# Kernel tuning notes

Hardware: AMD Instinct MI355X
Metric: run time of the kernel (lower is better)

## Reference

```python
import jax, jax.numpy as jnp
import numpy as np

H, W = 8, 64
HK, WK = 7, 11
N = H * W            # 512 tokens
C = 512              # embed_dim
HEADS = 8
HD = C // HEADS      # 64
SCALE = HD ** -0.5
B = 32


def build_local_mask():
    # Faithful port of the build() mask construction.
    m = np.ones([N, H + HK - 1, W + WK - 1], dtype=np.int32)
    for h in range(H):
        for w in range(W):
            m[h * W + w, h:h + HK, w:w + WK] = 0
    m = m[:, HK // 2:H + HK // 2, WK // 2:W + WK // 2].reshape(-1, N).astype(bool)
    mask = np.where(m, -1e30, 0.0).astype(np.float32)
    return jnp.asarray(mask.reshape(1, 1, N, N))


def setup_inputs() -> dict:
    key = jax.random.key(0)
    k1, k2, k3, k4 = jax.random.split(key, 4)
    return {
        "x": jax.random.normal(k1, (B, N, C), dtype=jnp.float32),
        "w_qkv": jax.random.normal(k2, (C, 3 * C), dtype=jnp.float32) * (C ** -0.5),
        "w_proj": jax.random.normal(k3, (C, C), dtype=jnp.float32) * (C ** -0.5),
        "b_proj": jax.random.normal(k4, (C,), dtype=jnp.float32) * 0.01,
        "mask": build_local_mask(),
    }


def reference(x, w_qkv, w_proj, b_proj, mask):
    b = x.shape[0]
    qkv = x @ w_qkv                                   # [B, N, 3C]
    qkv = qkv.reshape(b, N, 3, HEADS, HD)
    qkv = jnp.transpose(qkv, (2, 0, 3, 1, 4))          # [3, B, heads, N, hd]
    q, k, v = qkv[0], qkv[1], qkv[2]
    attn = jnp.einsum("bhnd,bhmd->bhnm", q * SCALE, k) + mask  # [B, heads, N, N]
    attn = jax.nn.softmax(attn, axis=-1)
    out = jnp.einsum("bhnm,bhmd->bhnd", attn, v)       # [B, heads, N, hd]
    out = jnp.transpose(out, (0, 2, 1, 3)).reshape(b, N, C)
    return out @ w_proj + b_proj
```

## Files before the change

### kernel.cpp

```cpp
#include <hip/hip_runtime.h>
#include <hip/hip_bf16.h>

typedef __attribute__((ext_vector_type(8))) __bf16 bf16x8;
typedef __attribute__((ext_vector_type(4))) float f32x4;

__device__ __forceinline__ unsigned short f2bf(float f) {
    unsigned int u = __float_as_uint(f);
    unsigned int r = u + 0x7FFFu + ((u >> 16) & 1u);
    return (unsigned short)(r >> 16);
}

__device__ __forceinline__ void async_copy16(const unsigned short* g, unsigned short* l) {
    __builtin_amdgcn_global_load_lds(
        (__attribute__((address_space(1))) void*)(g),
        (__attribute__((address_space(3))) void*)(l), 16, 0, 0);
}

__global__ __launch_bounds__(256) void cvt_f32_bf16(const float4* __restrict__ in,
                                                    uint4* __restrict__ out, int n8) {
    int i = blockIdx.x * blockDim.x + threadIdx.x;
    if (i >= n8) return;
    float4 a = in[2 * i], b = in[2 * i + 1];
    union { unsigned short s[8]; uint4 v; } r;
    r.s[0] = f2bf(a.x); r.s[1] = f2bf(a.y); r.s[2] = f2bf(a.z); r.s[3] = f2bf(a.w);
    r.s[4] = f2bf(b.x); r.s[5] = f2bf(b.y); r.s[6] = f2bf(b.z); r.s[7] = f2bf(b.w);
    out[i] = r.v;
}

__global__ __launch_bounds__(256) void transpose_cvt(const float* __restrict__ in,
                                                     unsigned short* __restrict__ out,
                                                     int R, int C) {
    __shared__ float tile[32][33];
    int c0 = blockIdx.x * 32, r0 = blockIdx.y * 32;
    int tx = threadIdx.x, ty = threadIdx.y;
    #pragma unroll
    for (int i = 0; i < 32; i += 8)
        tile[ty + i][tx] = in[(size_t)(r0 + ty + i) * C + c0 + tx];
    __syncthreads();
    #pragma unroll
    for (int i = 0; i < 32; i += 8)
        out[(size_t)(c0 + ty + i) * R + r0 + tx] = f2bf(tile[tx][ty + i]);
}

template <int K>
__device__ __forceinline__ void gemm_core_128_db(const unsigned short* __restrict__ A,
                                                 const unsigned short* __restrict__ Bt,
                                                 int m0, int n0, f32x4 acc[4][4]) {
    __shared__ unsigned short As[2][128 * 64];
    __shared__ unsigned short Bs[2][128 * 64];
    const int tid = threadIdx.x;
    const int lane = tid & 63;
    const int wv   = tid >> 6;
    const int wm = (wv >> 1) * 64, wn = (wv & 1) * 64;
    const int l15 = lane & 15, l16 = lane >> 4;

    f32x4 zz = {0.f, 0.f, 0.f, 0.f};
    #pragma unroll
    for (int i = 0; i < 4; ++i)
        #pragma unroll
        for (int j = 0; j < 4; ++j) acc[i][j] = zz;

    const int r_st  = tid >> 3;
    const int kk_st = (tid & 7) * 8;
    const unsigned short* Arow = A  + (size_t)(m0 + r_st) * K + kk_st;
    const unsigned short* Brow = Bt + (size_t)(n0 + r_st) * K + kk_st;

    #pragma unroll
    for (int c = 0; c < 4; ++c) {
        int flat16 = c * 256 + tid;
        async_copy16(Arow + (size_t)c * 32 * K, As[0] + flat16 * 8);
        async_copy16(Brow + (size_t)c * 32 * K, Bs[0] + flat16 * 8);
    }
    __syncthreads();

    constexpr int NT = K >> 6;
    #pragma unroll
    for (int t = 0; t < NT; ++t) {
        const int cur = t & 1;
        if (t + 1 < NT) {
            const int k0 = (t + 1) << 6;
            #pragma unroll
            for (int c = 0; c < 4; ++c) {
                int flat16 = c * 256 + tid;
                async_copy16(Arow + (size_t)c * 32 * K + k0, As[cur ^ 1] + flat16 * 8);
                async_copy16(Brow + (size_t)c * 32 * K + k0, Bs[cur ^ 1] + flat16 * 8);
            }
        }
        #pragma unroll
        for (int kk = 0; kk < 64; kk += 32) {
            bf16x8 a[4], b[4];
            #pragma unroll
            for (int i = 0; i < 4; ++i)
                a[i] = *(const bf16x8*)(const void*)(As[cur] + (wm + i * 16 + l15) * 64 + kk + l16 * 8);
            #pragma unroll
            for (int i = 0; i < 4; ++i)
                b[i] = *(const bf16x8*)(const void*)(Bs[cur] + (wn + i * 16 + l15) * 64 + kk + l16 * 8);
            #pragma unroll
            for (int i = 0; i < 4; ++i)
                #pragma unroll
                for (int j = 0; j < 4; ++j)
                    acc[i][j] = __builtin_amdgcn_mfma_f32_16x16x32_bf16(a[i], b[j], acc[i][j], 0, 0, 0);
        }
        __syncthreads();
    }
}

__global__ __launch_bounds__(256) void gemm_qkv(const unsigned short* __restrict__ xb,
                                                const unsigned short* __restrict__ wT,
                                                unsigned short* __restrict__ Qb,
                                                unsigned short* __restrict__ Kb,
                                                unsigned short* __restrict__ Vb) {
    f32x4 acc[4][4];
    int m0 = blockIdx.y * 128, n0 = blockIdx.x * 128;
    gemm_core_128_db<512>(xb, wT, m0, n0, acc);
    const int lane = threadIdx.x & 63, wv = threadIdx.x >> 6;
    const int wm = (wv >> 1) * 64, wn = (wv & 1) * 64;
    const int l15 = lane & 15, l16 = lane >> 4;
    #pragma unroll
    for (int j = 0; j < 4; ++j) {
        int col = n0 + wn + j * 16 + l15;
        int t = col >> 9;
        int within = col & 511;
        int h = within >> 6, d = within & 63;
        unsigned short* dst = (t == 0) ? Qb : (t == 1) ? Kb : Vb;
        float scl = (t == 0) ? 0.125f : 1.0f;
        #pragma unroll
        for (int i = 0; i < 4; ++i)
            #pragma unroll
            for (int e = 0; e < 4; ++e) {
                int row = m0 + wm + i * 16 + (l16 << 2) + e;
                int b = row >> 9, n = row & 511;
                dst[(((size_t)b * 8 + h) * 512 + n) * 64 + d] = f2bf(acc[i][j][e] * scl);
            }
    }
}

__global__ __launch_bounds__(256, 4) void attn_kernel(const unsigned short* __restrict__ Qb,
                                                      const unsigned short* __restrict__ Kb,
                                                      const unsigned short* __restrict__ Vb,
                                                      unsigned short* __restrict__ Ob) {
    __shared__ unsigned short Ks[64 * 72];
    __shared__ unsigned short Vt[64 * 72];
    __shared__ unsigned short Ps[4 * 32 * 72];

    const int bh = blockIdx.x >> 2;
    const int qt = blockIdx.x & 3;
    const int tid = threadIdx.x;
    const int lane = tid & 63;
    const int wv = tid >> 6;
    const int l15 = lane & 15, l16 = lane >> 4;
    const int b = bh >> 3, h = bh & 7;

    const unsigned short* Qp = Qb + (size_t)bh * 512 * 64;
    const unsigned short* Kp = Kb + (size_t)bh * 512 * 64;
    const unsigned short* Vp = Vb + (size_t)bh * 512 * 64;
    unsigned short* Pw = Ps + wv * 32 * 72;

    const int qrow0 = qt * 128 + wv * 32;
    const int qh = qrow0 >> 6;
    const int wq0 = qrow0 & 63;
    const int dead_g = wq0 ? 0 : 3;

    unsigned int wbits = 0;
    {
        int qw[2] = { wq0 + l15, wq0 + 16 + l15 };
        #pragma unroll
        for (int qf = 0; qf < 2; ++qf)
            #pragma unroll
            for (int g = 0; g < 4; ++g)
                #pragma unroll
                for (int j = 0; j < 4; ++j) {
                    int kw = g * 16 + (l16 << 2) + j;
                    int dw = qw[qf] - kw; dw = dw < 0 ? -dw : dw;
                    wbits |= (dw <= 5 ? 1u : 0u) << (qf * 16 + g * 4 + j);
                }
    }

    bf16x8 bQ[2][2];
    #pragma unroll
    for (int qf = 0; qf < 2; ++qf)
        #pragma unroll
        for (int kf = 0; kf < 2; ++kf)
            bQ[qf][kf] = *(const bf16x8*)(const void*)(Qp + (size_t)(qrow0 + qf * 16 + l15) * 64 + kf * 32 + l16 * 8);

    f32x4 o[2][4];
    f32x4 zz = {0.f, 0.f, 0.f, 0.f};
    float mrow[2] = {-INFINITY, -INFINITY}, lrow[2] = {0.f, 0.f};
    #pragma unroll
    for (int qf = 0; qf < 2; ++qf)
        #pragma unroll
        for (int df = 0; df < 4; ++df) o[qf][df] = zz;

    for (int kh = 0; kh < 8; ++kh) {
        int dlo = kh - 2 * qt;
        if (dlo < -3 || dlo > 4) continue;
        __syncthreads();
        #pragma unroll
        for (int c = 0; c < 2; ++c) {
            int flat16 = c * 256 + tid;
            int key = flat16 >> 3, dk = (flat16 & 7) * 8;
            *(uint4*)(void*)(Ks + key * 72 + dk) = *(const uint4*)(const void*)(Kp + ((size_t)(kh * 64 + key) * 64 + dk));
        }
        #pragma unroll
        for (int c = 0; c < 2; ++c) {
            int flat16 = c * 256 + tid;
            int key = flat16 & 63, d8 = flat16 >> 6;
            union { uint4 v; unsigned short s[8]; } t;
            t.v = *(const uint4*)(const void*)(Vp + ((size_t)(kh * 64 + key) * 64 + d8 * 8));
            #pragma unroll
            for (int e = 0; e < 8; ++e) Vt[(d8 * 8 + e) * 72 + key] = t.s[e];
        }
        __syncthreads();

        int adq = qh - kh; adq = adq < 0 ? -adq : adq;
        if (adq > 3) continue;

        f32x4 s[2][4];
        #pragma unroll
        for (int qf = 0; qf < 2; ++qf)
            #pragma unroll
            for (int g = 0; g < 4; ++g) s[qf][g] = zz;
        #pragma unroll
        for (int g = 0; g < 4; ++g) {
            if (g == dead_g) continue;
            bf16x8 aK0 = *(const bf16x8*)(const void*)(Ks + (g * 16 + l15) * 72 + 0  + l16 * 8);
            bf16x8 aK1 = *(const bf16x8*)(const void*)(Ks + (g * 16 + l15) * 72 + 32 + l16 * 8);
            #pragma unroll
            for (int qf = 0; qf < 2; ++qf) {
                s[qf][g] = __builtin_amdgcn_mfma_f32_16x16x32_bf16(aK0, bQ[qf][0], s[qf][g], 0, 0, 0);
                s[qf][g] = __builtin_amdgcn_mfma_f32_16x16x32_bf16(aK1, bQ[qf][1], s[qf][g], 0, 0, 0);
            }
        }

        float tmax[2] = {-1e30f, -1e30f};
        #pragma unroll
        for (int qf = 0; qf < 2; ++qf) {
            #pragma unroll
            for (int g = 0; g < 4; ++g) {
                if (g == dead_g) continue;
                #pragma unroll
                for (int j = 0; j < 4; ++j) {
                    float v = ((wbits >> (qf * 16 + g * 4 + j)) & 1u) ? s[qf][g][j] : -1e30f;
                    s[qf][g][j] = v;
                    tmax[qf] = fmaxf(tmax[qf], v);
                }
            }
            float t = tmax[qf];
            t = fmaxf(t, __shfl_xor(t, 16));
            t = fmaxf(t, __shfl_xor(t, 32));
            tmax[qf] = t;
        }

        #pragma unroll
        for (int qf = 0; qf < 2; ++qf) {
            float mnew = fmaxf(mrow[qf], tmax[qf]);
            float fs = __expf(mrow[qf] - mnew);
            mrow[qf] = mnew;
            lrow[qf] *= fs;
            #pragma unroll
            for (int j = 0; j < 4; ++j) {
                float fso = __shfl(fs, (l16 << 2) + j);
                #pragma unroll
                for (int df = 0; df < 4; ++df) o[qf][df][j] *= fso;
            }
        }

        #pragma unroll
        for (int qf = 0; qf < 2; ++qf) {
            float lsum = 0.f;
            #pragma unroll
            for (int g = 0; g < 4; ++g) {
                unsigned int lo, hi;
                if (g == dead_g) {
                    lo = 0u; hi = 0u;
                } else {
                    float e0 = __expf(s[qf][g][0] - mrow[qf]);
                    float e1 = __expf(s[qf][g][1] - mrow[qf]);
                    float e2 = __expf(s[qf][g][2] - mrow[qf]);
                    float e3 = __expf(s[qf][g][3] - mrow[qf]);
                    lsum += (e0 + e1) + (e2 + e3);
                    asm("v_cvt_pk_bf16_f32 %0, %1, %2" : "=v"(lo) : "v"(e0), "v"(e1));
                    asm("v_cvt_pk_bf16_f32 %0, %1, %2" : "=v"(hi) : "v"(e2), "v"(e3));
                }
                uint2 w; w.x = lo; w.y = hi;
                *(uint2*)(void*)(Pw + (qf * 16 + l15) * 72 + g * 16 + (l16 << 2)) = w;
            }
            float t = lsum;
            t += __shfl_xor(t, 16);
            t += __shfl_xor(t, 32);
            lrow[qf] += t;
        }
        asm volatile("" ::: "memory");

        #pragma unroll
        for (int kf = 0; kf < 2; ++kf) {
            bf16x8 aP0 = *(const bf16x8*)(const void*)(Pw + (0 * 16 + l15) * 72 + kf * 32 + l16 * 8);
            bf16x8 aP1 = *(const bf16x8*)(const void*)(Pw + (1 * 16 + l15) * 72 + kf * 32 + l16 * 8);
            #pragma unroll
            for (int df = 0; df < 4; ++df) {
                bf16x8 bV = *(const bf16x8*)(const void*)(Vt + (df * 16 + l15) * 72 + kf * 32 + l16 * 8);
                o[0][df] = __builtin_amdgcn_mfma_f32_16x16x32_bf16(aP0, bV, o[0][df], 0, 0, 0);
                o[1][df] = __builtin_amdgcn_mfma_f32_16x16x32_bf16(aP1, bV, o[1][df], 0, 0, 0);
            }
        }
    }

    #pragma unroll
    for (int qf = 0; qf < 2; ++qf) {
        float linv = 1.0f / lrow[qf];
        #pragma unroll
        for (int j = 0; j < 4; ++j) {
            float lj = __shfl(linv, (l16 << 2) + j);
            int q = qrow0 + qf * 16 + (l16 << 2) + j;
            size_t base = ((size_t)b * 512 + q) * 512 + h * 64;
            #pragma unroll
            for (int df = 0; df < 4; ++df)
                Ob[base + df * 16 + l15] = f2bf(o[qf][df][j] * lj);
        }
    }
}

__global__ __launch_bounds__(256) void gemm_proj(const unsigned short* __restrict__ Ab,
                                                 const unsigned short* __restrict__ wT,
                                                 const float* __restrict__ bias,
                                                 float* __restrict__ out) {
    f32x4 acc[4][4];
    int m0 = blockIdx.y * 128, n0 = blockIdx.x * 128;
    gemm_core_128_db<512>(Ab, wT, m0, n0, acc);
    const int lane = threadIdx.x & 63, wv = threadIdx.x >> 6;
    const int wm = (wv >> 1) * 64, wn = (wv & 1) * 64;
    const int l15 = lane & 15, l16 = lane >> 4;
    #pragma unroll
    for (int j = 0; j < 4; ++j) {
        int col = n0 + wn + j * 16 + l15;
        float bb = bias[col];
        #pragma unroll
        for (int i = 0; i < 4; ++i)
            #pragma unroll
            for (int e = 0; e < 4; ++e) {
                int row = m0 + wm + i * 16 + (l16 << 2) + e;
                out[(size_t)row * 512 + col] = acc[i][j][e] + bb;
            }
    }
}

extern "C" void kernel_launch(void* const* d_in, const int* in_sizes, int n_in,
                              void* d_out, int out_size, void* d_ws, size_t ws_size,
                              hipStream_t stream) {
    const float* x      = (const float*)d_in[0];
    const float* w_qkv  = (const float*)d_in[1];
    const float* w_proj = (const float*)d_in[2];
    const float* b_proj = (const float*)d_in[3];
    float* out = (float*)d_out;

    char* ws = (char*)d_ws;
    unsigned short* xb     = (unsigned short*)(ws);
    unsigned short* wqkvT  = (unsigned short*)(ws + 16777216);
    unsigned short* wprojT = (unsigned short*)(ws + 18350080);
    unsigned short* Qb     = (unsigned short*)(ws + 18874368);
    unsigned short* Kb     = (unsigned short*)(ws + 35651584);
    unsigned short* Vb     = (unsigned short*)(ws + 52428800);
    unsigned short* Ob     = xb;

    cvt_f32_bf16<<<4096, 256, 0, stream>>>((const float4*)x, (uint4*)xb, 1048576);
    transpose_cvt<<<dim3(48, 16), dim3(32, 8), 0, stream>>>(w_qkv, wqkvT, 512, 1536);
    transpose_cvt<<<dim3(16, 16), dim3(32, 8), 0, stream>>>(w_proj, wprojT, 512, 512);
    gemm_qkv<<<dim3(12, 128), 256, 0, stream>>>(xb, wqkvT, Qb, Kb, Vb);
    attn_kernel<<<1024, 256, 0, stream>>>(Qb, Kb, Vb, Ob);
    gemm_proj<<<dim3(4, 128), 256, 0, stream>>>(Ob, wprojT, b_proj, out);
}
```

Baseline: 114.6 us.

## Use 256x128 GEMM tiles with 8 waves, XCD-aware block mapping, interleaved prefetch

Both projection GEMMs now use one shared core with 256x128 tiles and 512 threads (8 waves, each computing a 64x64 sub-tile). Block indices are remapped so that each XCD handles a contiguous range of M tiles, which should improve L2 reuse of the A rows. The next K-tile is prefetched in four slices interleaved with the MFMA quarters, and s_setprio raises priority around the MFMA bursts. The larger tile uses more LDS and gives fewer blocks, which could lower occupancy.

```diff
diff --git a/kernel.cpp b/kernel.cpp
--- a/kernel.cpp
+++ b/kernel.cpp
@@ -42,83 +42,110 @@
         out[(size_t)(c0 + ty + i) * R + r0 + tx] = f2bf(tile[tx][ty + i]);
 }
 
-template <int K>
-__device__ __forceinline__ void gemm_core_128_db(const unsigned short* __restrict__ A,
-                                                 const unsigned short* __restrict__ Bt,
-                                                 int m0, int n0, f32x4 acc[4][4]) {
-    __shared__ unsigned short As[2][128 * 64];
+__device__ __forceinline__ void gemm_core_ph(const unsigned short* __restrict__ A,
+                                             const unsigned short* __restrict__ Bt,
+                                             int m0, int n0, f32x4 acc[4][4]) {
+    constexpr int K = 512, NT = 8;
+    __shared__ unsigned short As[2][256 * 64];
     __shared__ unsigned short Bs[2][128 * 64];
-    const int tid = threadIdx.x;
+
+    const int tid  = (int)threadIdx.x;
     const int lane = tid & 63;
     const int wv   = tid >> 6;
-    const int wm = (wv >> 1) * 64, wn = (wv & 1) * 64;
+    const int wr   = wv >> 1, wc = wv & 1;
+    const int l15  = lane & 15, l16 = lane >> 4;
+
+    const int r64 = tid >> 3;
+    const int kc  = (tid & 7) * 8;
+
+    f32x4 zz = {0.f, 0.f, 0.f, 0.f};
+    #pragma unroll
+    for (int i = 0; i < 4; ++i)
+        #pragma unroll
+        for (int j = 0; j < 4; ++j) acc[i][j] = zz;
+
+    #pragma unroll
+    for (int u = 0; u < 4; ++u)
+        async_copy16(A + (size_t)(m0 + u * 64 + r64) * K + kc,
+                     As[0] + (u * 64 + r64) * 64 + kc);
+    #pragma unroll
+    for (int u = 0; u < 2; ++u)
+        async_copy16(Bt + (size_t)(n0 + u * 64 + r64) * K + kc,
+                     Bs[0] + (u * 64 + r64) * 64 + kc);
+    __syncthreads();
+
+    for (int kt = 0; kt < NT; ++kt) {
+        const int slot = kt & 1;
+        const unsigned short* Ar = As[slot];
+        const unsigned short* Br = Bs[slot];
+        unsigned short* Aw = As[slot ^ 1];
+        unsigned short* Bw = Bs[slot ^ 1];
+        const int k1 = (kt + 1) * 64;
+        const bool more = (kt + 1 < NT);
+
+        #pragma unroll
+        for (int q = 0; q < 4; ++q) {
+            if (more) {
+                if (q == 0) {
+                    async_copy16(A + (size_t)(m0 + 0 * 64 + r64) * K + k1 + kc, Aw + (0 * 64 + r64) * 64 + kc);
+                    async_copy16(A + (size_t)(m0 + 1 * 64 + r64) * K + k1 + kc, Aw + (1 * 64 + r64) * 64 + kc);
+                } else if (q == 1) {
+                    async_copy16(A + (size_t)(m0 + 2 * 64 + r64) * K + k1 + kc, Aw + (2 * 64 + r64) * 64 + kc);
+                    async_copy16(A + (size_t)(m0 + 3 * 64 + r64) * K + k1 + kc, Aw + (3 * 64 + r64) * 64 + kc);
+                } else if (q == 2) {
+                    async_copy16(Bt + (size_t)(n0 + 0 * 64 + r64) * K + k1 + kc, Bw + (0 * 64 + r64) * 64 + kc);
+                } else {
+                    async_copy16(Bt + (size_t)(n0 + 1 * 64 + r64) * K + k1 + kc, Bw + (1 * 64 + r64) * 64 + kc);
+                }
+            }
+            const int qm = q >> 1, qn = q & 1;
+            bf16x8 a[2][2], b[2][2];
+            #pragma unroll
+            for (int i = 0; i < 2; ++i)
+                #pragma unroll
+                for (int kk = 0; kk < 2; ++kk)
+                    a[i][kk] = *(const bf16x8*)(const void*)(Ar + (wr * 64 + (qm * 2 + i) * 16 + l15) * 64 + kk * 32 + l16 * 8);
+            #pragma unroll
+            for (int j = 0; j < 2; ++j)
+                #pragma unroll
+                for (int kk = 0; kk < 2; ++kk)
+                    b[j][kk] = *(const bf16x8*)(const void*)(Br + (wc * 64 + (qn * 2 + j) * 16 + l15) * 64 + kk * 32 + l16 * 8);
+            __builtin_amdgcn_s_setprio(1);
+            #pragma unroll
+            for (int kk = 0; kk < 2; ++kk)
+                #pragma unroll
+                for (int i = 0; i < 2; ++i)
+                    #pragma unroll
+                    for (int j = 0; j < 2; ++j)
+                        acc[qm * 2 + i][qn * 2 + j] =
+                            __builtin_amdgcn_mfma_f32_16x16x32_bf16(a[i][kk], b[j][kk],
+                                                                    acc[qm * 2 + i][qn * 2 + j], 0, 0, 0);
+            __builtin_amdgcn_s_setprio(0);
+        }
+        __syncthreads();
+    }
+}
+
+__global__ __launch_bounds__(512) void gemm_qkv_ph(const unsigned short* __restrict__ xb,
+                                                   const unsigned short* __restrict__ wT,
+                                                   unsigned short* __restrict__ Qb,
+                                                   unsigned short* __restrict__ Kb,
+                                                   unsigned short* __restrict__ Vb) {
+    const int bid = blockIdx.x;
+    const int xcd = bid & 7, idx = bid >> 3;
+    const int mt  = xcd * 8 + idx / 12;
+    const int nt  = idx % 12;
+    const int m0 = mt * 256, n0 = nt * 128;
+
+    f32x4 acc[4][4];
+    gemm_core_ph(xb, wT, m0, n0, acc);
+
+    const int lane = (int)threadIdx.x & 63, wv = (int)threadIdx.x >> 6;
+    const int wr = wv >> 1, wc = wv & 1;
     const int l15 = lane & 15, l16 = lane >> 4;
-
-    f32x4 zz = {0.f, 0.f, 0.f, 0.f};
-    #pragma unroll
-    for (int i = 0; i < 4; ++i)
-        #pragma unroll
-        for (int j = 0; j < 4; ++j) acc[i][j] = zz;
-
-    const int r_st  = tid >> 3;
-    const int kk_st = (tid & 7) * 8;
-    const unsigned short* Arow = A  + (size_t)(m0 + r_st) * K + kk_st;
-    const unsigned short* Brow = Bt + (size_t)(n0 + r_st) * K + kk_st;
-
-    #pragma unroll
-    for (int c = 0; c < 4; ++c) {
-        int flat16 = c * 256 + tid;
-        async_copy16(Arow + (size_t)c * 32 * K, As[0] + flat16 * 8);
-        async_copy16(Brow + (size_t)c * 32 * K, Bs[0] + flat16 * 8);
-    }
-    __syncthreads();
-
-    constexpr int NT = K >> 6;
-    #pragma unroll
-    for (int t = 0; t < NT; ++t) {
-        const int cur = t & 1;
-        if (t + 1 < NT) {
-            const int k0 = (t + 1) << 6;
-            #pragma unroll
-            for (int c = 0; c < 4; ++c) {
-                int flat16 = c * 256 + tid;
-                async_copy16(Arow + (size_t)c * 32 * K + k0, As[cur ^ 1] + flat16 * 8);
-                async_copy16(Brow + (size_t)c * 32 * K + k0, Bs[cur ^ 1] + flat16 * 8);
-            }
-        }
-        #pragma unroll
-        for (int kk = 0; kk < 64; kk += 32) {
-            bf16x8 a[4], b[4];
-            #pragma unroll
-            for (int i = 0; i < 4; ++i)
-                a[i] = *(const bf16x8*)(const void*)(As[cur] + (wm + i * 16 + l15) * 64 + kk + l16 * 8);
-            #pragma unroll
-            for (int i = 0; i < 4; ++i)
-                b[i] = *(const bf16x8*)(const void*)(Bs[cur] + (wn + i * 16 + l15) * 64 + kk + l16 * 8);
-            #pragma unroll
-            for (int i = 0; i < 4; ++i)
-                #pragma unroll
-                for (int j = 0; j < 4; ++j)
-                    acc[i][j] = __builtin_amdgcn_mfma_f32_16x16x32_bf16(a[i], b[j], acc[i][j], 0, 0, 0);
-        }
-        __syncthreads();
-    }
-}
-
-__global__ __launch_bounds__(256) void gemm_qkv(const unsigned short* __restrict__ xb,
-                                                const unsigned short* __restrict__ wT,
-                                                unsigned short* __restrict__ Qb,
-                                                unsigned short* __restrict__ Kb,
-                                                unsigned short* __restrict__ Vb) {
-    f32x4 acc[4][4];
-    int m0 = blockIdx.y * 128, n0 = blockIdx.x * 128;
-    gemm_core_128_db<512>(xb, wT, m0, n0, acc);
-    const int lane = threadIdx.x & 63, wv = threadIdx.x >> 6;
-    const int wm = (wv >> 1) * 64, wn = (wv & 1) * 64;
-    const int l15 = lane & 15, l16 = lane >> 4;
     #pragma unroll
     for (int j = 0; j < 4; ++j) {
-        int col = n0 + wn + j * 16 + l15;
+        int col = n0 + wc * 64 + j * 16 + l15;
         int t = col >> 9;
         int within = col & 511;
         int h = within >> 6, d = within & 63;
@@ -128,9 +155,39 @@
         for (int i = 0; i < 4; ++i)
             #pragma unroll
             for (int e = 0; e < 4; ++e) {
-                int row = m0 + wm + i * 16 + (l16 << 2) + e;
+                int row = m0 + wr * 64 + i * 16 + (l16 << 2) + e;
                 int b = row >> 9, n = row & 511;
                 dst[(((size_t)b * 8 + h) * 512 + n) * 64 + d] = f2bf(acc[i][j][e] * scl);
+            }
+    }
+}
+
+__global__ __launch_bounds__(512) void gemm_proj_ph(const unsigned short* __restrict__ Ab,
+                                                    const unsigned short* __restrict__ wT,
+                                                    const float* __restrict__ bias,
+                                                    float* __restrict__ out) {
+    const int bid = blockIdx.x;
+    const int xcd = bid & 7, idx = bid >> 3;
+    const int mt  = xcd * 8 + idx / 4;
+    const int nt  = idx % 4;
+    const int m0 = mt * 256, n0 = nt * 128;
+
+    f32x4 acc[4][4];
+    gemm_core_ph(Ab, wT, m0, n0, acc);
+
+    const int lane = (int)threadIdx.x & 63, wv = (int)threadIdx.x >> 6;
+    const int wr = wv >> 1, wc = wv & 1;
+    const int l15 = lane & 15, l16 = lane >> 4;
+    #pragma unroll
+    for (int j = 0; j < 4; ++j) {
+        int col = n0 + wc * 64 + j * 16 + l15;
+        float bb = bias[col];
+        #pragma unroll
+        for (int i = 0; i < 4; ++i)
+            #pragma unroll
+            for (int e = 0; e < 4; ++e) {
+                int row = m0 + wr * 64 + i * 16 + (l16 << 2) + e;
+                out[(size_t)row * 512 + col] = acc[i][j][e] + bb;
             }
     }
 }
@@ -320,30 +377,6 @@
     }
 }
 
-__global__ __launch_bounds__(256) void gemm_proj(const unsigned short* __restrict__ Ab,
-                                                 const unsigned short* __restrict__ wT,
-                                                 const float* __restrict__ bias,
-                                                 float* __restrict__ out) {
-    f32x4 acc[4][4];
-    int m0 = blockIdx.y * 128, n0 = blockIdx.x * 128;
-    gemm_core_128_db<512>(Ab, wT, m0, n0, acc);
-    const int lane = threadIdx.x & 63, wv = threadIdx.x >> 6;
-    const int wm = (wv >> 1) * 64, wn = (wv & 1) * 64;
-    const int l15 = lane & 15, l16 = lane >> 4;
-    #pragma unroll
-    for (int j = 0; j < 4; ++j) {
-        int col = n0 + wn + j * 16 + l15;
-        float bb = bias[col];
-        #pragma unroll
-        for (int i = 0; i < 4; ++i)
-            #pragma unroll
-            for (int e = 0; e < 4; ++e) {
-                int row = m0 + wm + i * 16 + (l16 << 2) + e;
-                out[(size_t)row * 512 + col] = acc[i][j][e] + bb;
-            }
-    }
-}
-
 extern "C" void kernel_launch(void* const* d_in, const int* in_sizes, int n_in,
                               void* d_out, int out_size, void* d_ws, size_t ws_size,
                               hipStream_t stream) {
@@ -365,7 +398,7 @@
     cvt_f32_bf16<<<4096, 256, 0, stream>>>((const float4*)x, (uint4*)xb, 1048576);
     transpose_cvt<<<dim3(48, 16), dim3(32, 8), 0, stream>>>(w_qkv, wqkvT, 512, 1536);
     transpose_cvt<<<dim3(16, 16), dim3(32, 8), 0, stream>>>(w_proj, wprojT, 512, 512);
-    gemm_qkv<<<dim3(12, 128), 256, 0, stream>>>(xb, wqkvT, Qb, Kb, Vb);
+    gemm_qkv_ph<<<768, 512, 0, stream>>>(xb, wqkvT, Qb, Kb, Vb);
     attn_kernel<<<1024, 256, 0, stream>>>(Qb, Kb, Vb, Ob);
-    gemm_proj<<<dim3(4, 128), 256, 0, stream>>>(Ob, wprojT, b_proj, out);
-}
+    gemm_proj_ph<<<256, 512, 0, stream>>>(Ob, wprojT, b_proj, out);
+}
```

Result: slower. 135.0 us (+17.7%).
